# Optimization experiments

Hardware: AMD Instinct MI355X
Metric: run time of the kernel (lower is better)

The kernel has to match this reference:

```python
import jax, jax.numpy as jnp
import numpy as np

B, T, H, W, D = 32, 16, 32, 32, 64
N = T * H * W            # num_tokens = 16384
NUM_ELEMENTS = N * D     # world.num_elements
ALPHA = 1.0
EPS = 1e-6


def setup_inputs() -> dict:
    key = jax.random.key(0)
    k1, k2, k3, k4, k5, k6 = jax.random.split(key, 6)
    # uniforms feeding the gumbel noise
    u_g = jax.random.uniform(k1, (B, N), minval=EPS, maxval=1.0 - EPS, dtype=jnp.float32)
    # dirichlet marginal log-probs per axis (matches torch._sample_dirichlet().log())
    logp_t = jnp.log(jax.random.dirichlet(k2, jnp.full((T,), ALPHA), (B,)).astype(jnp.float32))
    logp_h = jnp.log(jax.random.dirichlet(k3, jnp.full((H,), ALPHA), (B,)).astype(jnp.float32))
    logp_w = jnp.log(jax.random.dirichlet(k4, jnp.full((W,), ALPHA), (B,)).astype(jnp.float32))
    # single uniform for the stratified masking rates
    u_k = jax.random.uniform(k5, (1,), dtype=jnp.float32)
    # per-element CRPS score (stand-in for loss_fn(tokens, ensemble), which is external)
    score = jax.random.uniform(k6, (B, N, D), dtype=jnp.float32)
    return {"u_g": u_g, "logp_t": logp_t, "logp_h": logp_h,
            "logp_w": logp_w, "u_k": u_k, "score": score}


def reference(u_g, logp_t, logp_h, logp_w, u_k, score):
    # get_visible_ws: gumbel noise + sum of dirichlet marginals broadcast over (t h w)
    gumbel = -jnp.log(-jnp.log(u_g))                                   # [B, N]
    marg = (logp_t[:, :, None, None]
            + logp_h[:, None, :, None]
            + logp_w[:, None, None, :]).reshape(B, N)                  # [B, N]
    ws = gumbel + marg

    # get_visible_ks: stratified rates -> k per row, clamped to [1, N-1]
    strat = jnp.linspace(0.0, 1.0, B, dtype=ws.dtype)
    rates = (u_k[0] + strat) % 1.0
    ks = jnp.clip((N * rates).astype(jnp.int32), 1, N - 1)             # [B]

    # binary_topk: rank of each token in descending order; visible = rank < k
    order = jnp.argsort(-ws, axis=-1)        # descending argsort        [B, N]
    ranks = jnp.argsort(order, axis=-1)      # inverse permutation       [B, N]
    visible = ranks < ks[:, None]            # bool                      [B, N]

    # masked, rate-corrected loss (land_sea_mask is None branch)
    mask = jnp.broadcast_to(~visible[:, :, None], score.shape).astype(score.dtype)  # [B, N, D]
    rate_correction = jnp.sum(mask, axis=(1, 2), keepdims=True) / NUM_ELEMENTS      # [B, 1, 1]
    loss = jnp.mean(score * mask / rate_correction)
    return loss, visible
```

## Files before the change

### kernel.cpp

```cpp
#include <hip/hip_runtime.h>
#include <hip/hip_bf16.h>

#define B_   32
#define T_   16
#define H_   32
#define W_   32
#define D_   64
#define N_   16384
#define BLK  256
#define BLK_S 1024
#define SEG_  8
#define KPT_A 2
#define KPT_S 16
#define LOSS_BLOCKS 2048
#define LOSS_ITERS  16
#define CAP 2048
#define NBIN 2048

__global__ __launch_bounds__(BLK_S, 1) void select_a_kernel(
    const float* __restrict__ u_g,
    const float* __restrict__ logp_t,
    const float* __restrict__ logp_h,
    const float* __restrict__ logp_w,
    unsigned* __restrict__ keys_out,
    unsigned* __restrict__ hist_out)
{
    const int ba  = blockIdx.x;
    const int b   = ba >> 3;
    const int sg  = ba & 7;
    const int tid = threadIdx.x;

    __shared__ float s_lt[T_], s_lh[H_], s_lw[W_];
    __shared__ unsigned s_hist[NBIN];

    if (tid < T_) s_lt[tid] = logp_t[b*T_ + tid];
    if (tid < H_) s_lh[tid] = logp_h[b*H_ + tid];
    if (tid < W_) s_lw[tid] = logp_w[b*W_ + tid];
    s_hist[tid]        = 0u;
    s_hist[tid + 1024] = 0u;
    __syncthreads();

#pragma unroll
    for (int i = 0; i < KPT_A; ++i) {
        int   n = sg*(N_/SEG_) + i*BLK_S + tid;
        float u = u_g[b*N_ + n];
        float g = -logf(-logf(u));
        int t = n >> 10;
        int h = (n >> 5) & 31;
        int w = n & 31;
        float wsv = g + ((s_lt[t] + s_lh[h]) + s_lw[w]);
        unsigned bits = __float_as_uint(wsv);
        unsigned key  = (bits & 0x80000000u) ? ~bits : (bits | 0x80000000u);
        keys_out[b*N_ + n] = key;
        atomicAdd(&s_hist[key >> 21], 1u);
    }
    __syncthreads();

    hist_out[ba*NBIN + tid]        = s_hist[tid];
    hist_out[ba*NBIN + tid + 1024] = s_hist[tid + 1024];
}

__global__ __launch_bounds__(BLK_S, 1) void select_b_kernel(
    unsigned* keybuf,
    const unsigned* __restrict__ hist_in,
    const float* __restrict__ u_k,
    double* __restrict__ invrc)
{
    const int b    = blockIdx.x;
    const int tid  = threadIdx.x;
    const int lane = tid & 63;
    const int wv   = tid >> 6;

    __shared__ unsigned s_hist2[NBIN];
    __shared__ unsigned s_wsum[16];
    __shared__ int s_bucket, s_above, s_cnt;
    __shared__ unsigned s_thr;
    __shared__ int s_cgt, s_ceq;
    __shared__ unsigned long long s_list[CAP];

    s_hist2[tid]        = 0u;
    s_hist2[tid + 1024] = 0u;
    if (tid == 0) s_cnt = 0;

    unsigned h0 = 0, h1 = 0;
    {
        const uint2* hb2 = (const uint2*)(hist_in + (size_t)b*SEG_*NBIN);
#pragma unroll
        for (int j = 0; j < SEG_; ++j) {
            uint2 v = hb2[j*(NBIN/2) + tid];
            h0 += v.x; h1 += v.y;
        }
    }

    unsigned keys[KPT_S];
#pragma unroll
    for (int i = 0; i < KPT_S; ++i)
        keys[i] = keybuf[b*N_ + i*BLK_S + tid];

    float u0    = u_k[0];
    float strat = (b == B_-1) ? 1.0f : (float)((double)b * (1.0/31.0));
    float rate  = fmodf(u0 + strat, 1.0f);
    int   k     = (int)(16384.0f * rate);
    k = k < 1 ? 1 : (k > N_-1 ? N_-1 : k);

    {
        const unsigned p = h0 + h1;
        unsigned x = p;
#pragma unroll
        for (int off = 1; off < 64; off <<= 1) {
            unsigned y = __shfl_down(x, off);
            if (lane + off < 64) x += y;
        }
        if (lane == 0) s_wsum[wv] = x;
        __syncthreads();
        unsigned wsuf = 0;
#pragma unroll
        for (int w2 = 0; w2 < 16; ++w2) wsuf += (w2 > wv) ? s_wsum[w2] : 0u;
        const unsigned sufExcl = (x - p) + wsuf;
        const unsigned ku = (unsigned)k;
        const unsigned a1 = sufExcl;
        const unsigned a0 = sufExcl + h1;
        if (a1 < ku && ku <= a1 + h1) { s_bucket = 2*tid + 1; s_above = (int)a1; }
        if (a0 < ku && ku <= a0 + h0) { s_bucket = 2*tid;     s_above = (int)a0; }
        __syncthreads();
    }

    const int bucket = s_bucket;
    const int above  = s_above;
    const int need   = k - above;

#pragma unroll
    for (int i = 0; i < KPT_S; ++i) {
        if ((int)(keys[i] >> 21) == bucket)
            atomicAdd(&s_hist2[(keys[i] >> 10) & 0x7FFu], 1u);
    }
    __syncthreads();

    {
        const unsigned g0 = s_hist2[2*tid];
        const unsigned g1 = s_hist2[2*tid + 1];
        const unsigned p  = g0 + g1;
        unsigned x = p;
#pragma unroll
        for (int off = 1; off < 64; off <<= 1) {
            unsigned y = __shfl_down(x, off);
            if (lane + off < 64) x += y;
        }
        if (lane == 0) s_wsum[wv] = x;
        __syncthreads();
        unsigned wsuf = 0;
#pragma unroll
        for (int w2 = 0; w2 < 16; ++w2) wsuf += (w2 > wv) ? s_wsum[w2] : 0u;
        const unsigned sufExcl = (x - p) + wsuf;
        const unsigned ku = (unsigned)need;
        const unsigned a1 = sufExcl;
        const unsigned a0 = sufExcl + g1;
        if (a1 < ku && ku <= a1 + g1) { s_bucket = 2*tid + 1; s_above = (int)a1; }
        if (a0 < ku && ku <= a0 + g0) { s_bucket = 2*tid;     s_above = (int)a0; }
        __syncthreads();
    }

    const int bucket2 = s_bucket;
    const int above2  = s_above;
    const int need2   = need - above2;
    const unsigned pfx22 = ((unsigned)bucket << 11) | (unsigned)bucket2;

#pragma unroll
    for (int i = 0; i < KPT_S; ++i) {
        if ((keys[i] >> 10) == pfx22) {
            int slot = atomicAdd(&s_cnt, 1);
            if (slot < CAP)
                s_list[slot] = ((unsigned long long)keys[i] << 32)
                             | (unsigned)(i*BLK_S + tid);
        }
    }
    __syncthreads();

    const int M = s_cnt < CAP ? s_cnt : CAP;
    for (int i = tid; i < M; i += BLK_S) {
        const unsigned ki = (unsigned)(s_list[i] >> 32);
        int gt = 0, eq = 0;
        for (int j = 0; j < M; ++j) {
            const unsigned kj = (unsigned)(s_list[j] >> 32);
            gt += (kj > ki) ? 1 : 0;
            eq += (kj == ki) ? 1 : 0;
        }
        if (gt < need2 && need2 <= gt + eq) {
            s_thr = ki;
            s_cgt = above + above2 + gt;
            s_ceq = eq;
        }
    }
    __syncthreads();

    const unsigned thr = s_thr;
    const int count_gt = s_cgt;
    const int count_eq = s_ceq;
    const int need_eq  = k - count_gt;
    const bool rare    = (count_eq != need_eq);

#pragma unroll
    for (int i = 0; i < KPT_S; ++i) {
        int n = i*BLK_S + tid;
        float v;
        if (keys[i] > thr) {
            v = 1.0f;
        } else if (keys[i] == thr) {
            if (!rare || count_eq > CAP) {
                v = 1.0f;
            } else {
                int rk = 0;
                for (int j = 0; j < M; ++j) {
                    unsigned long long e = s_list[j];
                    rk += ((unsigned)(e >> 32) == thr &&
                           (int)(e & 0xFFFFFFFFull) < n) ? 1 : 0;
                }
                v = (rk < need_eq) ? 1.0f : 0.0f;
            }
        } else {
            v = 0.0f;
        }
        keybuf[b*N_ + n] = __float_as_uint(v);
    }

    if (tid == 0) {
        float rc = (float)(N_ - k) / (float)N_;
        invrc[b] = 1.0 / (double)rc;
    }
}

__global__ __launch_bounds__(BLK, 1) void loss_kernel(
    const float*  __restrict__ score,
    const float*  __restrict__ vis,
    const double* __restrict__ invrc,
    double*       __restrict__ partial)
{
    const int tid = threadIdx.x;
    __shared__ double s_w[B_];
    if (tid < B_) s_w[tid] = invrc[tid];
    __syncthreads();

    const int gtid = blockIdx.x * BLK + tid;
    const int NT   = LOSS_BLOCKS * BLK;
    const float4* s4 = (const float4*)score;

    float vm[LOSS_ITERS];
#pragma unroll
    for (int i = 0; i < LOSS_ITERS; ++i)
        vm[i] = vis[(gtid + i * NT) >> 4];

    double a = 0.0;
#pragma unroll
    for (int i = 0; i < LOSS_ITERS; ++i) {
        int f = gtid + i * NT;
        if (vm[i] == 0.0f) {
            float4 x = s4[f];
            float  s = (x.x + x.y) + (x.z + x.w);
            a += (double)s * s_w[f >> 18];
        }
    }

    for (int off = 32; off > 0; off >>= 1) a += __shfl_down(a, off);
    __shared__ double s_a[4];
    if ((tid & 63) == 0) s_a[tid >> 6] = a;
    __syncthreads();
    if (tid == 0) partial[blockIdx.x] = s_a[0] + s_a[1] + s_a[2] + s_a[3];
}

__global__ __launch_bounds__(BLK, 1) void finalize_kernel(
    const double* __restrict__ partial,
    float* __restrict__ out)
{
    const int tid = threadIdx.x;
    double t = 0.0;
    for (int i = tid; i < LOSS_BLOCKS; i += BLK) t += partial[i];
    for (int off = 32; off > 0; off >>= 1) t += __shfl_down(t, off);
    __shared__ double s_a[4];
    if ((tid & 63) == 0) s_a[tid >> 6] = t;
    __syncthreads();
    if (tid == 0)
        out[0] = (float)((s_a[0] + s_a[1] + s_a[2] + s_a[3]) / 33554432.0);
}

extern "C" void kernel_launch(void* const* d_in, const int* in_sizes, int n_in,
                              void* d_out, int out_size, void* d_ws, size_t ws_size,
                              hipStream_t stream) {
    const float* u_g    = (const float*)d_in[0];
    const float* logp_t = (const float*)d_in[1];
    const float* logp_h = (const float*)d_in[2];
    const float* logp_w = (const float*)d_in[3];
    const float* u_k    = (const float*)d_in[4];
    const float* score  = (const float*)d_in[5];

    float*  out     = (float*)d_out;
    double* wsd     = (double*)d_ws;
    double*   invrc   = wsd;
    double*   partial = wsd + B_;
    unsigned* histbuf = (unsigned*)(wsd + B_ + LOSS_BLOCKS + 8);
    unsigned* keybuf  = (unsigned*)(out + 1);

    select_a_kernel<<<B_*SEG_, BLK_S, 0, stream>>>(u_g, logp_t, logp_h, logp_w,
                                                   keybuf, histbuf);
    select_b_kernel<<<B_, BLK_S, 0, stream>>>(keybuf, histbuf, u_k, invrc);
    loss_kernel<<<LOSS_BLOCKS, BLK, 0, stream>>>(score, (const float*)keybuf,
                                                 invrc, partial);
    finalize_kernel<<<1, BLK, 0, stream>>>(partial, out);
}
```

Before: 34.52 us.

## Compact masked token indices in select_b and gather only masked rows in loss

select_b now builds a per-batch prefix-sum compacted list of masked token indices and a count. It writes them into the reused histogram workspace. The loss kernel then gathers only those tokens' score rows, 16 lanes per 256-byte row, with one weight per block. This removes the dense visibility scan and the divergent skipped loads, and spreads the masked work evenly across blocks. The cost is a scan and scattered list writes in select_b, and it relies on the masked count being exactly N-k.

```diff
diff --git a/kernel.cpp b/kernel.cpp
--- a/kernel.cpp
+++ b/kernel.cpp
@@ -13,7 +13,6 @@
 #define KPT_A 2
 #define KPT_S 16
 #define LOSS_BLOCKS 2048
-#define LOSS_ITERS  16
 #define CAP 2048
 #define NBIN 2048
 
@@ -62,9 +61,10 @@
 
 __global__ __launch_bounds__(BLK_S, 1) void select_b_kernel(
     unsigned* keybuf,
-    const unsigned* __restrict__ hist_in,
+    unsigned* histlist,
     const float* __restrict__ u_k,
-    double* __restrict__ invrc)
+    double* __restrict__ invrc,
+    unsigned* __restrict__ cnt_out)
 {
     const int b    = blockIdx.x;
     const int tid  = threadIdx.x;
@@ -84,7 +84,7 @@
 
     unsigned h0 = 0, h1 = 0;
     {
-        const uint2* hb2 = (const uint2*)(hist_in + (size_t)b*SEG_*NBIN);
+        const uint2* hb2 = (const uint2*)(histlist + (size_t)b*SEG_*NBIN);
 #pragma unroll
         for (int j = 0; j < SEG_; ++j) {
             uint2 v = hb2[j*(NBIN/2) + tid];
@@ -199,6 +199,7 @@
     const int need_eq  = k - count_gt;
     const bool rare    = (count_eq != need_eq);
 
+    unsigned mbits = 0u;
 #pragma unroll
     for (int i = 0; i < KPT_S; ++i) {
         int n = i*BLK_S + tid;
@@ -220,43 +221,68 @@
         } else {
             v = 0.0f;
         }
+        if (v == 0.0f) mbits |= (1u << i);
         keybuf[b*N_ + n] = __float_as_uint(v);
     }
 
+    const int myc = (int)__popc(mbits);
+    int xs = myc;
+#pragma unroll
+    for (int off = 1; off < 64; off <<= 1) {
+        int y = __shfl_up(xs, off);
+        if (lane >= off) xs += y;
+    }
+    if (lane == 63) s_wsum[wv] = (unsigned)xs;
+    __syncthreads();
+    int wpre = 0;
+#pragma unroll
+    for (int w2 = 0; w2 < 16; ++w2) wpre += (w2 < wv) ? (int)s_wsum[w2] : 0;
+    unsigned off0 = (unsigned)(wpre + xs - myc);
+    unsigned* mylist = histlist + (size_t)b*SEG_*NBIN;
+#pragma unroll
+    for (int i = 0; i < KPT_S; ++i) {
+        if (mbits & (1u << i))
+            mylist[off0++] = (unsigned)(b*N_ + i*BLK_S + tid);
+    }
+
     if (tid == 0) {
+        cnt_out[b] = (unsigned)(N_ - k);
         float rc = (float)(N_ - k) / (float)N_;
         invrc[b] = 1.0 / (double)rc;
     }
 }
 
 __global__ __launch_bounds__(BLK, 1) void loss_kernel(
-    const float*  __restrict__ score,
-    const float*  __restrict__ vis,
+    const float4* __restrict__ s4,
+    const unsigned* __restrict__ list,
+    const unsigned* __restrict__ cnt,
     const double* __restrict__ invrc,
     double*       __restrict__ partial)
 {
     const int tid = threadIdx.x;
-    __shared__ double s_w[B_];
-    if (tid < B_) s_w[tid] = invrc[tid];
-    __syncthreads();
-
-    const int gtid = blockIdx.x * BLK + tid;
-    const int NT   = LOSS_BLOCKS * BLK;
-    const float4* s4 = (const float4*)score;
-
-    float vm[LOSS_ITERS];
-#pragma unroll
-    for (int i = 0; i < LOSS_ITERS; ++i)
-        vm[i] = vis[(gtid + i * NT) >> 4];
+    const int g   = tid >> 4;
+    const int l   = tid & 15;
+    const int bid = blockIdx.x;
+    const int b   = bid >> 6;
+    const int j0  = bid & 63;
+    const int m   = (int)cnt[b];
+    const unsigned* ml = list + (size_t)b*N_;
+    const double w = invrc[b];
+
+    unsigned gt[16];
+#pragma unroll
+    for (int s = 0; s < 16; ++s) {
+        int slot = (s*64 + j0)*16 + g;
+        gt[s] = (slot < m) ? ml[slot] : 0xFFFFFFFFu;
+    }
 
     double a = 0.0;
 #pragma unroll
-    for (int i = 0; i < LOSS_ITERS; ++i) {
-        int f = gtid + i * NT;
-        if (vm[i] == 0.0f) {
-            float4 x = s4[f];
-            float  s = (x.x + x.y) + (x.z + x.w);
-            a += (double)s * s_w[f >> 18];
+    for (int s = 0; s < 16; ++s) {
+        if (gt[s] != 0xFFFFFFFFu) {
+            float4 x = s4[(size_t)gt[s]*16 + l];
+            float  sv = (x.x + x.y) + (x.z + x.w);
+            a += (double)sv * w;
         }
     }
 
@@ -264,7 +290,7 @@
     __shared__ double s_a[4];
     if ((tid & 63) == 0) s_a[tid >> 6] = a;
     __syncthreads();
-    if (tid == 0) partial[blockIdx.x] = s_a[0] + s_a[1] + s_a[2] + s_a[3];
+    if (tid == 0) partial[bid] = s_a[0] + s_a[1] + s_a[2] + s_a[3];
 }
 
 __global__ __launch_bounds__(BLK, 1) void finalize_kernel(
@@ -296,13 +322,15 @@
     double* wsd     = (double*)d_ws;
     double*   invrc   = wsd;
     double*   partial = wsd + B_;
-    unsigned* histbuf = (unsigned*)(wsd + B_ + LOSS_BLOCKS + 8);
+    unsigned* cntbuf  = (unsigned*)(wsd + B_ + LOSS_BLOCKS);
+    unsigned* histbuf = (unsigned*)(wsd + B_ + LOSS_BLOCKS + 16);
     unsigned* keybuf  = (unsigned*)(out + 1);
 
     select_a_kernel<<<B_*SEG_, BLK_S, 0, stream>>>(u_g, logp_t, logp_h, logp_w,
                                                    keybuf, histbuf);
-    select_b_kernel<<<B_, BLK_S, 0, stream>>>(keybuf, histbuf, u_k, invrc);
-    loss_kernel<<<LOSS_BLOCKS, BLK, 0, stream>>>(score, (const float*)keybuf,
-                                                 invrc, partial);
+    select_b_kernel<<<B_, BLK_S, 0, stream>>>(keybuf, histbuf, u_k, invrc,
+                                              cntbuf);
+    loss_kernel<<<LOSS_BLOCKS, BLK, 0, stream>>>((const float4*)score, histbuf,
+                                                 cntbuf, invrc, partial);
     finalize_kernel<<<1, BLK, 0, stream>>>(partial, out);
 }
```

Result: slower. 41.62 us (+20.6%).
